# Performance work log

Hardware: AMD Instinct MI355X
Metric: run time of the kernel (lower is better)

The kernel has to match this reference:

```python
import jax, jax.numpy as jnp
import numpy as np


def setup_inputs() -> dict:
    key = jax.random.key(0)
    kq, kk, kv = jax.random.split(key, 3)
    B, L, H, D = 2, 4096, 8, 64
    queries = jax.random.normal(kq, (B, L, H, D), dtype=jnp.float32)
    keys = jax.random.normal(kk, (B, L, H, D), dtype=jnp.float32)
    values = jax.random.normal(kv, (B, L, H, D), dtype=jnp.float32)
    return {"queries": queries, "keys": keys, "values": values}


def reference(queries, keys, values):
    # queries/keys/values: [B, L, H, D]
    d_model = queries.shape[-1]
    scale = 1.0 / jnp.sqrt(jnp.asarray(d_model, dtype=queries.dtype))
    # scores: [B, H, Lq, Lk]
    scores = jnp.einsum('blhd,bshd->bhls', queries, keys)
    # dropout is identity in eval mode / for deterministic reference
    A = jax.nn.softmax(scale * scores, axis=-1)
    # output: [B, Lq, H, D]
    V = jnp.einsum('bhls,bshd->blhd', A, values)
    return V
```

## Files before the change

kernel.cpp:

```cpp
#include <hip/hip_runtime.h>

#define Bn 2
#define Ln 4096
#define Hn 8
#define Dn 64
#define NMEGA 32
#define BH_STRIDE 262144

typedef float    f32x4  __attribute__((ext_vector_type(4)));
typedef float    f32x16 __attribute__((ext_vector_type(16)));
typedef _Float16 f16x2  __attribute__((ext_vector_type(2)));
typedef _Float16 f16x8  __attribute__((ext_vector_type(8)));
typedef unsigned int u32;
typedef u32 u32x2 __attribute__((ext_vector_type(2)));
typedef u32 u32x4 __attribute__((ext_vector_type(4)));

static __device__ __forceinline__ u32 pkf16(float a, float b){
    auto h = __builtin_amdgcn_cvt_pkrtz(a, b);
    return __builtin_bit_cast(u32, h);
}

static __device__ __forceinline__ u32x2 swp(u32 a, u32 b){
    auto r = __builtin_amdgcn_permlane32_swap(a, b, false, false);
    return __builtin_bit_cast(u32x2, r);
}

__global__ __launch_bounds__(256)
void kvprep(const float* __restrict__ Kg, const float* __restrict__ Vg,
            _Float16* __restrict__ kp, _Float16* __restrict__ vp){
    __shared__ float tV[64*65];
    const int t = blockIdx.x, bh = blockIdx.y, b = bh>>3, h = bh&7;
    const int tid = threadIdx.x;
#pragma unroll
    for(int i=0;i<4;++i){
        int idx = tid + i*256;
        int k = idx >> 4, d4 = (idx & 15)*4;
        float4 v = *(const float4*)(Vg + (((size_t)b*Ln + t*64 + k)*Hn + h)*Dn + d4);
        tV[k*65+d4+0]=v.x; tV[k*65+d4+1]=v.y;
        tV[k*65+d4+2]=v.z; tV[k*65+d4+3]=v.w;
    }
#pragma unroll
    for(int i=0;i<2;++i){
        int u = tid + i*256;
        int lane = u & 63, unit = u >> 6;
        int g = unit >> 2, cc = unit & 3;
        const float* src = Kg + (((size_t)b*Ln + t*64 + g*32 + (lane&31))*Hn + h)*Dn
                         + cc*16 + (lane>>5)*8;
        float4 a = *(const float4*)src;
        float4 c4 = *(const float4*)(src + 4);
        f16x8 o;
        o[0]=(_Float16)a.x;  o[1]=(_Float16)a.y;  o[2]=(_Float16)a.z;  o[3]=(_Float16)a.w;
        o[4]=(_Float16)c4.x; o[5]=(_Float16)c4.y; o[6]=(_Float16)c4.z; o[7]=(_Float16)c4.w;
        *(f16x8*)(kp + (size_t)bh*BH_STRIDE + (size_t)t*4096 + (size_t)u*8) = o;
    }
    __syncthreads();
#pragma unroll
    for(int i=0;i<2;++i){
        int u = tid + i*256;
        int lane = u & 63, unit = u >> 6;
        int g = unit >> 2, kh = (unit >> 1) & 1, dt = unit & 1;
        int krow = g*32 + kh*16 + (lane>>5)*8;
        int d = dt*32 + (lane&31);
        f16x8 o;
#pragma unroll
        for(int j=0;j<8;++j) o[j] = (_Float16)tV[(krow+j)*65 + d];
        *(f16x8*)(vp + (size_t)bh*BH_STRIDE + (size_t)t*4096 + (size_t)u*8) = o;
    }
}

static __device__ __forceinline__ f32x16 qk4(const f16x8 (&kf)[4], const f16x8 (&qf)[4]){
    f32x16 s;
#pragma unroll
    for(int r=0;r<16;++r) s[r]=0.f;
    s = __builtin_amdgcn_mfma_f32_32x32x16_f16(kf[0], qf[0], s, 0,0,0);
    s = __builtin_amdgcn_mfma_f32_32x32x16_f16(kf[1], qf[1], s, 0,0,0);
    s = __builtin_amdgcn_mfma_f32_32x32x16_f16(kf[2], qf[2], s, 0,0,0);
    s = __builtin_amdgcn_mfma_f32_32x32x16_f16(kf[3], qf[3], s, 0,0,0);
    return s;
}

static __device__ __forceinline__ void finish_pv(const f32x16& S, float& lac,
                                                 f32x16& o0, f32x16& o1,
                                                 const f16x8 (&vf)[4]){
    f32x16 p;
#pragma unroll
    for(int r=0;r<16;++r) p[r] = __builtin_amdgcn_exp2f(S[r]);
    u32 A0 = pkf16(p[0],p[1]),   A1 = pkf16(p[2],p[3]);
    u32 B0 = pkf16(p[4],p[5]),   B1 = pkf16(p[6],p[7]);
    u32 C0 = pkf16(p[8],p[9]),   C1 = pkf16(p[10],p[11]);
    u32 D0 = pkf16(p[12],p[13]), D1 = pkf16(p[14],p[15]);
    u32x2 r0 = swp(A0,B0), r1 = swp(A1,B1);
    u32x2 r2 = swp(C0,D0), r3 = swp(C1,D1);
    u32x4 w0 = {r0.x, r1.x, r0.y, r1.y};
    u32x4 w1 = {r2.x, r3.x, r2.y, r3.y};
    f16x8 pa0 = __builtin_bit_cast(f16x8, w0);
    f16x8 pa1 = __builtin_bit_cast(f16x8, w1);
    const f16x2 ones = {(_Float16)1.0f, (_Float16)1.0f};
#pragma unroll
    for(int j=0;j<4;++j){
        f16x2 c0 = {pa0[2*j], pa0[2*j+1]};
        f16x2 c1 = {pa1[2*j], pa1[2*j+1]};
        lac = __builtin_amdgcn_fdot2(c0, ones, lac, false);
        lac = __builtin_amdgcn_fdot2(c1, ones, lac, false);
    }
    o0 = __builtin_amdgcn_mfma_f32_32x32x16_f16(pa0, vf[0], o0, 0,0,0);
    o0 = __builtin_amdgcn_mfma_f32_32x32x16_f16(pa1, vf[2], o0, 0,0,0);
    o1 = __builtin_amdgcn_mfma_f32_32x32x16_f16(pa0, vf[1], o1, 0,0,0);
    o1 = __builtin_amdgcn_mfma_f32_32x32x16_f16(pa1, vf[3], o1, 0,0,0);
}

static __device__ __forceinline__ void ld4(f16x8 (&dst)[4], const char* base, int off){
#pragma unroll
    for(int i=0;i<4;++i) dst[i] = *(const f16x8*)(base + ((off+i)<<10));
}

__global__ __launch_bounds__(512,2)
void attn_fwd(const float* __restrict__ Qg, float* __restrict__ Og,
              const _Float16* __restrict__ kp, const _Float16* __restrict__ vp){
    __shared__ __align__(16) float xo[4*32*64 + 128];

    const int tid  = threadIdx.x;
    const int lane = tid & 63, wv = tid >> 6;
    const int kh2 = wv & 1, qh = wv >> 1;
    const int l31 = lane & 31, hi = lane >> 5;
    const int bh = blockIdx.x, b = bh>>3, h = bh&7;
    const int q0 = blockIdx.y*128 + qh*32;

    const float c = 0.125f * 1.4426950408889634f;

    f16x8 qf[4];
    {
        const float* qrow = Qg + (((size_t)b*Ln + q0 + l31)*Hn + h)*Dn;
#pragma unroll
        for(int cc=0;cc<4;++cc){
            const float* p4 = qrow + cc*16 + hi*8;
            float4 x = *(const float4*)p4;
            float4 y = *(const float4*)(p4+4);
            f16x8 f;
            f[0]=(_Float16)(x.x*c); f[1]=(_Float16)(x.y*c);
            f[2]=(_Float16)(x.z*c); f[3]=(_Float16)(x.w*c);
            f[4]=(_Float16)(y.x*c); f[5]=(_Float16)(y.y*c);
            f[6]=(_Float16)(y.z*c); f[7]=(_Float16)(y.w*c);
            qf[cc]=f;
        }
    }

    f32x16 o0, o1;
    float lac = 0.f;
#pragma unroll
    for(int r=0;r<16;++r){ o0[r]=0.f; o1[r]=0.f; }

    const char* kgc = (const char*)(kp + (size_t)bh*BH_STRIDE) + kh2*8192 + lane*16;
    const char* vgc = (const char*)(vp + (size_t)bh*BH_STRIDE) + kh2*8192 + lane*16;

    for(int T=0; T<NMEGA; ++T){
        const char* Kb = kgc + (size_t)T*16384;
        const char* Vb = vgc + (size_t)T*16384;

        f16x8 kf0[4], vf0[4];
        ld4(kf0, Kb, 0); ld4(vf0, Vb, 0);
        f32x16 S0 = qk4(kf0, qf);

        f16x8 kf1[4], vf1[4];
        ld4(kf1, Kb, 4); ld4(vf1, Vb, 4);
        finish_pv(S0, lac, o0, o1, vf0);

        f32x16 S1 = qk4(kf1, qf);
        finish_pv(S1, lac, o0, o1, vf1);
    }

    float lred = lac + __shfl_xor(lac, 32, 64);

    float* xl = xo + 4*32*64;
    if(kh2){
#pragma unroll
        for(int r=0;r<16;++r){
            int qr = (r&3) + 8*(r>>2) + 4*hi;
            xo[(qh*32 + qr)*64 +  0 + l31] = o0[r];
            xo[(qh*32 + qr)*64 + 32 + l31] = o1[r];
        }
        if(hi==0) xl[qh*32 + l31] = lred;
    }
    __syncthreads();
    if(!kh2){
        float inv = 1.0f/(lred + xl[qh*32 + l31]);
        float* ob = Og + (((size_t)b*Ln + q0)*Hn + h)*Dn;
#pragma unroll
        for(int r=0;r<16;++r){
            int qr = (r&3) + 8*(r>>2) + 4*hi;
            float invr = __shfl(inv, qr, 64);
            float v0 = o0[r] + xo[(qh*32 + qr)*64 +  0 + l31];
            float v1 = o1[r] + xo[(qh*32 + qr)*64 + 32 + l31];
            ob[(size_t)qr*Hn*Dn +  0 + l31] = v0*invr;
            ob[(size_t)qr*Hn*Dn + 32 + l31] = v1*invr;
        }
    }
}

extern "C" void kernel_launch(void* const* d_in, const int* in_sizes, int n_in,
                              void* d_out, int out_size, void* d_ws, size_t ws_size,
                              hipStream_t stream) {
    const float* Q = (const float*)d_in[0];
    const float* K = (const float*)d_in[1];
    const float* V = (const float*)d_in[2];
    float* O = (float*)d_out;

    _Float16* kp = (_Float16*)d_ws;
    _Float16* vp = (_Float16*)((char*)d_ws + (8u<<20));

    kvprep<<<dim3(64, 16), dim3(256), 0, stream>>>(K, V, kp, vp);
    attn_fwd<<<dim3(16, 32), dim3(512), 0, stream>>>(Q, O, kp, vp);
}
```

Baseline: 202.5 us.

## Halve attention block size and drop shared-memory transpose in KV prep

The attention kernel now uses 256-thread blocks covering 64 queries instead of 512-thread blocks covering 128, which doubles the grid to 1024 blocks so the CUs are better filled and tail effects shrink. The KV prep kernel now gives each block 32 keys and reads V directly from global memory with strided loads, replacing the shared-memory transpose and barrier. The cost is that each K/V tile is read from global memory by twice as many attention blocks, and the V loads in prep are less coalesced.

```diff
diff --git a/kernel.cpp b/kernel.cpp
--- a/kernel.cpp
+++ b/kernel.cpp
@@ -28,43 +28,32 @@
 __global__ __launch_bounds__(256)
 void kvprep(const float* __restrict__ Kg, const float* __restrict__ Vg,
             _Float16* __restrict__ kp, _Float16* __restrict__ vp){
-    __shared__ float tV[64*65];
-    const int t = blockIdx.x, bh = blockIdx.y, b = bh>>3, h = bh&7;
+    const int t2 = blockIdx.x, bh = blockIdx.y, b = bh>>3, h = bh&7;
     const int tid = threadIdx.x;
-#pragma unroll
-    for(int i=0;i<4;++i){
-        int idx = tid + i*256;
-        int k = idx >> 4, d4 = (idx & 15)*4;
-        float4 v = *(const float4*)(Vg + (((size_t)b*Ln + t*64 + k)*Hn + h)*Dn + d4);
-        tV[k*65+d4+0]=v.x; tV[k*65+d4+1]=v.y;
-        tV[k*65+d4+2]=v.z; tV[k*65+d4+3]=v.w;
-    }
-#pragma unroll
-    for(int i=0;i<2;++i){
-        int u = tid + i*256;
-        int lane = u & 63, unit = u >> 6;
-        int g = unit >> 2, cc = unit & 3;
-        const float* src = Kg + (((size_t)b*Ln + t*64 + g*32 + (lane&31))*Hn + h)*Dn
-                         + cc*16 + (lane>>5)*8;
-        float4 a = *(const float4*)src;
-        float4 c4 = *(const float4*)(src + 4);
+    const int w = tid >> 6, lane = tid & 63;
+    const int l31 = lane & 31, hi = lane >> 5;
+    const int t = t2 >> 1, g = t2 & 1;
+
+    {
+        const float* ks = Kg + (((size_t)b*Ln + t2*32 + l31)*Hn + h)*Dn + w*16 + hi*8;
+        float4 a  = *(const float4*)ks;
+        float4 c4 = *(const float4*)(ks + 4);
         f16x8 o;
         o[0]=(_Float16)a.x;  o[1]=(_Float16)a.y;  o[2]=(_Float16)a.z;  o[3]=(_Float16)a.w;
         o[4]=(_Float16)c4.x; o[5]=(_Float16)c4.y; o[6]=(_Float16)c4.z; o[7]=(_Float16)c4.w;
-        *(f16x8*)(kp + (size_t)bh*BH_STRIDE + (size_t)t*4096 + (size_t)u*8) = o;
-    }
-    __syncthreads();
-#pragma unroll
-    for(int i=0;i<2;++i){
-        int u = tid + i*256;
-        int lane = u & 63, unit = u >> 6;
-        int g = unit >> 2, kh = (unit >> 1) & 1, dt = unit & 1;
-        int krow = g*32 + kh*16 + (lane>>5)*8;
-        int d = dt*32 + (lane&31);
+        *(f16x8*)(kp + (size_t)bh*BH_STRIDE + (size_t)t*4096
+                     + (size_t)(g*4 + w)*512 + (size_t)lane*8) = o;
+    }
+
+    {
+        const int kh = w >> 1, dt = w & 1;
+        const float* vs = Vg + (((size_t)b*Ln + t2*32 + kh*16 + hi*8)*Hn + h)*Dn
+                        + dt*32 + l31;
         f16x8 o;
 #pragma unroll
-        for(int j=0;j<8;++j) o[j] = (_Float16)tV[(krow+j)*65 + d];
-        *(f16x8*)(vp + (size_t)bh*BH_STRIDE + (size_t)t*4096 + (size_t)u*8) = o;
+        for(int j=0;j<8;++j) o[j] = (_Float16)vs[(size_t)j*Hn*Dn];
+        *(f16x8*)(vp + (size_t)bh*BH_STRIDE + (size_t)t*4096
+                     + (size_t)(g*4 + w)*512 + (size_t)lane*8) = o;
     }
 }
 
@@ -114,17 +103,17 @@
     for(int i=0;i<4;++i) dst[i] = *(const f16x8*)(base + ((off+i)<<10));
 }
 
-__global__ __launch_bounds__(512,2)
+__global__ __launch_bounds__(256,2)
 void attn_fwd(const float* __restrict__ Qg, float* __restrict__ Og,
               const _Float16* __restrict__ kp, const _Float16* __restrict__ vp){
-    __shared__ __align__(16) float xo[4*32*64 + 128];
+    __shared__ __align__(16) float xo[2*32*64 + 64];
 
     const int tid  = threadIdx.x;
     const int lane = tid & 63, wv = tid >> 6;
     const int kh2 = wv & 1, qh = wv >> 1;
     const int l31 = lane & 31, hi = lane >> 5;
     const int bh = blockIdx.x, b = bh>>3, h = bh&7;
-    const int q0 = blockIdx.y*128 + qh*32;
+    const int q0 = blockIdx.y*64 + qh*32;
 
     const float c = 0.125f * 1.4426950408889634f;
 
@@ -171,7 +160,7 @@
 
     float lred = lac + __shfl_xor(lac, 32, 64);
 
-    float* xl = xo + 4*32*64;
+    float* xl = xo + 2*32*64;
     if(kh2){
 #pragma unroll
         for(int r=0;r<16;++r){
@@ -208,6 +197,6 @@
     _Float16* kp = (_Float16*)d_ws;
     _Float16* vp = (_Float16*)((char*)d_ws + (8u<<20));
 
-    kvprep<<<dim3(64, 16), dim3(256), 0, stream>>>(K, V, kp, vp);
-    attn_fwd<<<dim3(16, 32), dim3(512), 0, stream>>>(Q, O, kp, vp);
-}
+    kvprep<<<dim3(128, 16), dim3(256), 0, stream>>>(K, V, kp, vp);
+    attn_fwd<<<dim3(16, 64), dim3(256), 0, stream>>>(Q, O, kp, vp);
+}
```

After: 202.1 us. No clear change (-0.2%).
